# Optimization experiments

Hardware: AMD Instinct MI355X
Metric: run time of the kernel (lower is better)

The kernel has to match this reference:

```python
import jax, jax.numpy as jnp
import numpy as np

N_NODES = 100000


def gcn_conv(x, W, b, src, dst, n):
    """PyG GCNConv: add self-loops, symmetric degree norm, linear, scatter-add."""
    loop = jnp.arange(n, dtype=src.dtype)
    s = jnp.concatenate([src, loop])  # source nodes (message origin)
    d = jnp.concatenate([dst, loop])  # target nodes (aggregation)
    deg = jax.ops.segment_sum(jnp.ones_like(d, dtype=x.dtype), d, num_segments=n)
    dinv = jnp.where(deg > 0, jax.lax.rsqrt(deg), 0.0)
    norm = dinv[s] * dinv[d]  # [E+N]
    h = x @ W  # [N, out]
    msg = h[s] * norm[:, None]  # [E+N, out]
    return jax.ops.segment_sum(msg, d, num_segments=n) + b


def setup_inputs() -> dict:
    key = jax.random.key(0)
    ks = jax.random.split(key, 8)
    n, e, din, dh, dout = N_NODES, 3200000, 128, 64, 6
    x = jax.random.normal(ks[0], (n, din), dtype=jnp.float32)
    edge_index = jax.random.randint(ks[1], (2, e), 0, n, dtype=jnp.int64)
    sc = lambda f: 1.0 / np.sqrt(f)
    W1 = jax.random.normal(ks[2], (din, dh), dtype=jnp.float32) * sc(din)
    b1 = jnp.zeros((dh,), dtype=jnp.float32)
    W2 = jax.random.normal(ks[3], (dh, dh), dtype=jnp.float32) * sc(dh)
    b2 = jnp.zeros((dh,), dtype=jnp.float32)
    W3 = jax.random.normal(ks[4], (dh, dout), dtype=jnp.float32) * sc(dh)
    b3 = jnp.zeros((dout,), dtype=jnp.float32)
    return {"x": x, "edge_index": edge_index, "W1": W1, "b1": b1,
            "W2": W2, "b2": b2, "W3": W3, "b3": b3}


def reference(x, edge_index, W1, b1, W2, b2, W3, b3):
    n = x.shape[0]
    src, dst = edge_index[0], edge_index[1]
    # eval mode: dropout is identity
    h = jax.nn.relu(gcn_conv(x, W1, b1, src, dst, n))
    h = jax.nn.relu(gcn_conv(h, W2, b2, src, dst, n))
    h = gcn_conv(h, W3, b3, src, dst, n)
    return jax.nn.log_softmax(h, axis=1)
```

## Files before the change

### kernel.cpp

```cpp
#include <hip/hip_runtime.h>
#include <hip/hip_fp16.h>
#include <math.h>


#define WS_ALIGN(x) (((x) + 255) & ~(size_t)255)
#define BKN 256
#define CAP 8960
#define EPT 16
#define BIN_THR 512
#define BIN_CHUNK (BIN_THR * EPT)

typedef _Float16 half8 __attribute__((ext_vector_type(8)));
typedef float floatx4 __attribute__((ext_vector_type(4)));

__global__ __launch_bounds__(BIN_THR) void bin_kernel(
    const int* __restrict__ src, const int* __restrict__ dst,
    int* __restrict__ cur, int* __restrict__ slab, int E, int NB) {
    __shared__ int counts[400];
    const int tid = threadIdx.x;
    const int base = blockIdx.x * BIN_CHUNK + tid * EPT;
    for (int i = tid; i < NB; i += BIN_THR) counts[i] = 0;
    __syncthreads();
    int b[EPT], w[EPT], lpos[EPT];
    #pragma unroll
    for (int k = 0; k < EPT; ++k) {
        int e = base + k;
        if (e < E) {
            int s = src[e], d = dst[e];
            b[k] = d >> 8;
            w[k] = (s << 8) | (d & 255);
        } else b[k] = -1;
    }
    #pragma unroll
    for (int k = 0; k < EPT; ++k)
        if (b[k] >= 0) lpos[k] = atomicAdd(&counts[b[k]], 1);
    __syncthreads();
    for (int i = tid; i < NB; i += BIN_THR) {
        int c = counts[i];
        counts[i] = c ? atomicAdd(&cur[i], c) : 0;
    }
    __syncthreads();
    #pragma unroll
    for (int k = 0; k < EPT; ++k) {
        if (b[k] >= 0) {
            int pos = counts[b[k]] + lpos[k];
            if (pos < CAP) slab[(size_t)b[k] * CAP + pos] = w[k];
        }
    }
}

__global__ __launch_bounds__(512) void bucket_sort_kernel(
    const int* __restrict__ slab, const int* __restrict__ cur,
    int* __restrict__ srcS, int* __restrict__ rowbeg, int* __restrict__ rowend,
    float* __restrict__ dinv, int n) {
    __shared__ int cnt[BKN], s[BKN], cursor[BKN];
    const int b = blockIdx.x, tid = threadIdx.x;
    const int m = min(cur[b], CAP);
    const int* sp = slab + (size_t)b * CAP;
    if (tid < BKN) cnt[tid] = 0;
    __syncthreads();
    for (int j = tid; j < m; j += 512) atomicAdd(&cnt[sp[j] & 255], 1);
    __syncthreads();
    if (tid < BKN) s[tid] = cnt[tid];
    __syncthreads();
    for (int off = 1; off < BKN; off <<= 1) {
        int v = 0;
        if (tid < BKN && tid >= off) v = s[tid - off];
        __syncthreads();
        if (tid < BKN) s[tid] += v;
        __syncthreads();
    }
    if (tid < BKN) {
        int ofs = s[tid] - cnt[tid];
        cursor[tid] = ofs;
        int node = b * BKN + tid;
        if (node < n) {
            rowbeg[node] = b * CAP + ofs;
            rowend[node] = b * CAP + ofs + cnt[tid];
            dinv[node] = rsqrtf((float)(cnt[tid] + 1));
        }
    }
    __syncthreads();
    for (int j = tid; j < m; j += 512) {
        int w = sp[j];
        int p = atomicAdd(&cursor[w & 255], 1);
        srcS[(size_t)b * CAP + p] = w >> 8;
    }
}

template <int K>
__global__ __launch_bounds__(256) void linear_mfma_f32_kernel(
    const float* __restrict__ Xf, const float* __restrict__ W,
    const float* __restrict__ dinv, _Float16* __restrict__ Y, int n) {
    constexpr int KC = K / 32;
    __shared__ _Float16 Bf[KC * 4 * 64 * 8];
    const int tid = threadIdx.x;
    for (int i = tid; i < KC * 4 * 64 * 8; i += 256) {
        int j = i & 7, lane = (i >> 3) & 63, tile = (i >> 9) & 3, kc = i >> 11;
        int k = kc * 32 + ((lane >> 4) << 3) + j;
        int col = tile * 16 + (lane & 15);
        Bf[i] = (_Float16)W[k * 64 + col];
    }
    __syncthreads();
    const int lane = tid & 63, wid = tid >> 6;
    const int base = blockIdx.x * 64 + wid * 16;
    if (base >= n) return;
    const int mrow = lane & 15, quad = lane >> 4;
    const int anode = min(base + mrow, n - 1);
    floatx4 acc[4] = {{0, 0, 0, 0}, {0, 0, 0, 0}, {0, 0, 0, 0}, {0, 0, 0, 0}};
    #pragma unroll
    for (int kc = 0; kc < KC; ++kc) {
        float4 xa = *(const float4*)&Xf[(size_t)anode * K + kc * 32 + quad * 8];
        float4 xb = *(const float4*)&Xf[(size_t)anode * K + kc * 32 + quad * 8 + 4];
        half8 a;
        a[0] = (_Float16)xa.x; a[1] = (_Float16)xa.y; a[2] = (_Float16)xa.z; a[3] = (_Float16)xa.w;
        a[4] = (_Float16)xb.x; a[5] = (_Float16)xb.y; a[6] = (_Float16)xb.z; a[7] = (_Float16)xb.w;
        #pragma unroll
        for (int t = 0; t < 4; ++t) {
            half8 b = *(const half8*)&Bf[((kc * 4 + t) * 64 + lane) * 8];
            acc[t] = __builtin_amdgcn_mfma_f32_16x16x32_f16(a, b, acc[t], 0, 0, 0);
        }
    }
    #pragma unroll
    for (int r = 0; r < 4; ++r) {
        int node = base + quad * 4 + r;
        if (node < n) {
            float di = dinv[node];
            #pragma unroll
            for (int t = 0; t < 4; ++t)
                Y[(size_t)node * 64 + t * 16 + mrow] = (_Float16)(acc[t][r] * di);
        }
    }
}

__global__ __launch_bounds__(256) void linear_mfma_f16_kernel(
    const _Float16* __restrict__ Xh, const float* __restrict__ W,
    const float* __restrict__ dinv, _Float16* __restrict__ Y, int n) {
    constexpr int K = 64, KC = 2;
    __shared__ _Float16 Bf[KC * 4 * 64 * 8];
    const int tid = threadIdx.x;
    for (int i = tid; i < KC * 4 * 64 * 8; i += 256) {
        int j = i & 7, lane = (i >> 3) & 63, tile = (i >> 9) & 3, kc = i >> 11;
        int k = kc * 32 + ((lane >> 4) << 3) + j;
        int col = tile * 16 + (lane & 15);
        Bf[i] = (_Float16)W[k * 64 + col];
    }
    __syncthreads();
    const int lane = tid & 63, wid = tid >> 6;
    const int base = blockIdx.x * 64 + wid * 16;
    if (base >= n) return;
    const int mrow = lane & 15, quad = lane >> 4;
    const int anode = min(base + mrow, n - 1);
    floatx4 acc[4] = {{0, 0, 0, 0}, {0, 0, 0, 0}, {0, 0, 0, 0}, {0, 0, 0, 0}};
    #pragma unroll
    for (int kc = 0; kc < KC; ++kc) {
        half8 a = *(const half8*)&Xh[(size_t)anode * K + kc * 32 + quad * 8];
        #pragma unroll
        for (int t = 0; t < 4; ++t) {
            half8 b = *(const half8*)&Bf[((kc * 4 + t) * 64 + lane) * 8];
            acc[t] = __builtin_amdgcn_mfma_f32_16x16x32_f16(a, b, acc[t], 0, 0, 0);
        }
    }
    #pragma unroll
    for (int r = 0; r < 4; ++r) {
        int node = base + quad * 4 + r;
        if (node < n) {
            float di = dinv[node];
            #pragma unroll
            for (int t = 0; t < 4; ++t)
                Y[(size_t)node * 64 + t * 16 + mrow] = (_Float16)(acc[t][r] * di);
        }
    }
}

__global__ __launch_bounds__(256) void linear3_kernel(const __half* __restrict__ Xh,
                                                      const float* __restrict__ W,
                                                      const float* __restrict__ dinv,
                                                      __half* __restrict__ Y, int n) {
    __shared__ float Wl[64 * 6];
    __shared__ float Xs[32][65];
    const int tid = threadIdx.x;
    for (int i = tid; i < 64 * 6; i += 256) Wl[i] = W[i];
    const int sub = tid >> 3;
    const int feat = tid & 7;
    for (int base = blockIdx.x * 32; base < n; base += gridDim.x * 32) {
        __syncthreads();
        for (int i = tid; i < 32 * 64; i += 256) {
            int r = i >> 6, c = i & 63;
            int node = base + r;
            Xs[r][c] = (node < n) ? __half2float(Xh[(size_t)node * 64 + c]) : 0.f;
        }
        __syncthreads();
        int node = base + sub;
        if (node < n) {
            float r = 0.f;
            if (feat < 6) {
                float acc = 0.f;
                #pragma unroll
                for (int k = 0; k < 64; ++k) acc = fmaf(Xs[sub][k], Wl[k * 6 + feat], acc);
                r = acc * dinv[node];
            }
            Y[(size_t)node * 8 + feat] = __float2half_rn(r);
        }
    }
}

__global__ __launch_bounds__(256) void agg64_kernel(
    const _Float16* __restrict__ Hs, const float* __restrict__ dinv,
    const int* __restrict__ srcS, const int* __restrict__ rowbeg,
    const int* __restrict__ rowend, const float* __restrict__ bias,
    _Float16* __restrict__ Out, int n, int do_relu) {
    const int wave = (blockIdx.x * blockDim.x + threadIdx.x) >> 6;
    const int lane = threadIdx.x & 63;
    if (wave >= n) return;
    const int slot = lane >> 3;
    const int f8 = lane & 7;
    const int beg = rowbeg[wave], end = rowend[wave];
    float acc[8] = {0.f, 0.f, 0.f, 0.f, 0.f, 0.f, 0.f, 0.f};
    int j = beg;
    for (; j + 16 <= end; j += 16) {
        int sA = srcS[j + slot];
        int sB = srcS[j + 8 + slot];
        half8 vA = *(const half8*)&Hs[(size_t)sA * 64 + f8 * 8];
        half8 vB = *(const half8*)&Hs[(size_t)sB * 64 + f8 * 8];
        #pragma unroll
        for (int i = 0; i < 8; ++i) acc[i] += (float)vA[i] + (float)vB[i];
    }
    for (; j < end; j += 8) {
        int jj = j + slot;
        int s = srcS[min(jj, end - 1)];
        half8 v = *(const half8*)&Hs[(size_t)s * 64 + f8 * 8];
        float flag = (jj < end) ? 1.f : 0.f;
        #pragma unroll
        for (int i = 0; i < 8; ++i) acc[i] = fmaf((float)v[i], flag, acc[i]);
    }
    #pragma unroll
    for (int i = 0; i < 8; ++i) {
        acc[i] += __shfl_xor(acc[i], 8);
        acc[i] += __shfl_xor(acc[i], 16);
        acc[i] += __shfl_xor(acc[i], 32);
    }
    half8 self = *(const half8*)&Hs[(size_t)wave * 64 + f8 * 8];
    const float di = dinv[wave];
    float4 b0 = *(const float4*)&bias[f8 * 8];
    float4 b1 = *(const float4*)&bias[f8 * 8 + 4];
    float bb[8] = {b0.x, b0.y, b0.z, b0.w, b1.x, b1.y, b1.z, b1.w};
    half8 o;
    #pragma unroll
    for (int i = 0; i < 8; ++i) {
        float v = (acc[i] + (float)self[i]) * di + bb[i];
        if (do_relu) v = fmaxf(v, 0.f);
        o[i] = (_Float16)v;
    }
    if (slot == 0) *(half8*)&Out[(size_t)wave * 64 + f8 * 8] = o;
}

__global__ __launch_bounds__(256) void agg6_lsm_kernel(
    const __half* __restrict__ Hs6, const float* __restrict__ dinv,
    const int* __restrict__ srcS, const int* __restrict__ rowbeg,
    const int* __restrict__ rowend, const float* __restrict__ bias,
    float* __restrict__ out, int n) {
    const int wave = (blockIdx.x * blockDim.x + threadIdx.x) >> 6;
    const int lane = threadIdx.x & 63;
    if (wave >= n) return;
    const int slot = lane >> 3, f = lane & 7;
    const int beg = rowbeg[wave], end = rowend[wave];
    float part = 0.f;
    for (int j0 = beg; j0 < end; j0 += 8) {
        int j = j0 + slot;
        if (j < end) part += __half2float(Hs6[(size_t)srcS[j] * 8 + f]);
    }
    part += __shfl_xor(part, 8);
    part += __shfl_xor(part, 16);
    part += __shfl_xor(part, 32);
    float bi = (f < 6) ? bias[f] : 0.f;
    float a = (part + __half2float(Hs6[(size_t)wave * 8 + f])) * dinv[wave] + bi;
    float am = (f < 6) ? a : -1e30f;
    float m = am;
    m = fmaxf(m, __shfl_xor(m, 1));
    m = fmaxf(m, __shfl_xor(m, 2));
    m = fmaxf(m, __shfl_xor(m, 4));
    float ex = (f < 6) ? expf(a - m) : 0.f;
    float sum = ex;
    sum += __shfl_xor(sum, 1);
    sum += __shfl_xor(sum, 2);
    sum += __shfl_xor(sum, 4);
    float lse = m + logf(sum);
    if (slot == 0 && f < 6) out[(size_t)wave * 6 + f] = a - lse;
}

extern "C" void kernel_launch(void* const* d_in, const int* in_sizes, int n_in,
                              void* d_out, int out_size, void* d_ws, size_t ws_size,
                              hipStream_t stream) {
    const float* x  = (const float*)d_in[0];
    const int*   ei = (const int*)d_in[1];
    const float* W1 = (const float*)d_in[2];
    const float* b1 = (const float*)d_in[3];
    const float* W2 = (const float*)d_in[4];
    const float* b2 = (const float*)d_in[5];
    const float* W3 = (const float*)d_in[6];
    const float* b3 = (const float*)d_in[7];
    float* out = (float*)d_out;

    const int n = in_sizes[0] / 128;
    const int E = in_sizes[1] / 2;
    const int* src = ei;
    const int* dst = ei + E;
    const int NB = (n + BKN - 1) / BKN;

    char* ws = (char*)d_ws;
    auto carve = [&](size_t bytes) { char* p = ws; ws += WS_ALIGN(bytes); return p; };
    int*      cur    = (int*)     carve((size_t)NB * 4);
    float*    dinv   = (float*)   carve((size_t)n * 4);
    int*      slab   = (int*)     carve((size_t)NB * CAP * 4);
    int*      srcS   = (int*)     carve((size_t)NB * CAP * 4);
    int*      rowbeg = (int*)     carve((size_t)n * 4);
    int*      rowend = (int*)     carve((size_t)n * 4);
    _Float16* hsA    = (_Float16*)carve((size_t)n * 64 * 2 + 4096);
    _Float16* hsB    = (_Float16*)carve((size_t)n * 64 * 2 + 4096);
    __half*   hsC    = (__half*)  carve((size_t)n * 8 * 2);
    (void)ws_size; (void)n_in; (void)out_size;

    hipMemsetAsync(cur, 0, (size_t)NB * 4, stream);
    bin_kernel<<<(E + BIN_CHUNK - 1) / BIN_CHUNK, BIN_THR, 0, stream>>>(src, dst, cur, slab, E, NB);
    bucket_sort_kernel<<<NB, 512, 0, stream>>>(slab, cur, srcS, rowbeg, rowend, dinv, n);

    const int aggGrid = (n + 3) / 4;
    const int linGrid = (n + 63) / 64;

    linear_mfma_f32_kernel<128><<<linGrid, 256, 0, stream>>>(x, W1, dinv, hsA, n);
    agg64_kernel<<<aggGrid, 256, 0, stream>>>(hsA, dinv, srcS, rowbeg, rowend, b1, hsB, n, 1);

    linear_mfma_f16_kernel<<<linGrid, 256, 0, stream>>>(hsB, W2, dinv, hsA, n);
    agg64_kernel<<<aggGrid, 256, 0, stream>>>(hsA, dinv, srcS, rowbeg, rowend, b2, hsB, n, 1);

    linear3_kernel<<<2048, 256, 0, stream>>>((const __half*)hsB, W3, dinv, hsC, n);
    agg6_lsm_kernel<<<aggGrid, 256, 0, stream>>>(hsC, dinv, srcS, rowbeg, rowend, b3, out, n);
}
```

Baseline: 374.3 us.

## Fuse layer-3 linear into second aggregation and accumulate gathers in fp16

Removes the separate linear3 kernel by folding the 64x6 projection into the second agg64 pass, using fp16 dot2 on weights staged in LDS plus a lane shuffle reduction. This drops one full read and write of the 64-wide hidden array. The gather accumulation also switches from fp32 to packed fp16 vector adds and fp16 shuffles, which cuts ALU work but lowers accumulation precision for high-degree nodes. The tail loop now uses a branch instead of the masked FMA.

New measurement: 375.1 us. Within noise of the previous version (+0.2%).

```diff
diff --git a/kernel.cpp b/kernel.cpp
--- a/kernel.cpp
+++ b/kernel.cpp
@@ -11,7 +11,21 @@
 #define BIN_CHUNK (BIN_THR * EPT)
 
 typedef _Float16 half8 __attribute__((ext_vector_type(8)));
+typedef _Float16 half2v __attribute__((ext_vector_type(2)));
 typedef float floatx4 __attribute__((ext_vector_type(4)));
+
+#if defined(__has_builtin)
+#if __has_builtin(__builtin_amdgcn_fdot2)
+#define HAVE_FDOT2 1
+#endif
+#endif
+static __device__ __forceinline__ float fdot2f(half2v a, half2v b, float c) {
+#ifdef HAVE_FDOT2
+    return __builtin_amdgcn_fdot2(a, b, c, false);
+#else
+    return c + (float)a[0] * (float)b[0] + (float)a[1] * (float)b[1];
+#endif
+}
 
 __global__ __launch_bounds__(BIN_THR) void bin_kernel(
     const int* __restrict__ src, const int* __restrict__ dst,
@@ -173,86 +187,107 @@
     }
 }
 
-__global__ __launch_bounds__(256) void linear3_kernel(const __half* __restrict__ Xh,
-                                                      const float* __restrict__ W,
-                                                      const float* __restrict__ dinv,
-                                                      __half* __restrict__ Y, int n) {
-    __shared__ float Wl[64 * 6];
-    __shared__ float Xs[32][65];
-    const int tid = threadIdx.x;
-    for (int i = tid; i < 64 * 6; i += 256) Wl[i] = W[i];
-    const int sub = tid >> 3;
-    const int feat = tid & 7;
-    for (int base = blockIdx.x * 32; base < n; base += gridDim.x * 32) {
-        __syncthreads();
-        for (int i = tid; i < 32 * 64; i += 256) {
-            int r = i >> 6, c = i & 63;
-            int node = base + r;
-            Xs[r][c] = (node < n) ? __half2float(Xh[(size_t)node * 64 + c]) : 0.f;
-        }
-        __syncthreads();
-        int node = base + sub;
-        if (node < n) {
-            float r = 0.f;
-            if (feat < 6) {
-                float acc = 0.f;
-                #pragma unroll
-                for (int k = 0; k < 64; ++k) acc = fmaf(Xs[sub][k], Wl[k * 6 + feat], acc);
-                r = acc * dinv[node];
-            }
-            Y[(size_t)node * 8 + feat] = __float2half_rn(r);
-        }
-    }
-}
-
+template <bool FUSE3>
 __global__ __launch_bounds__(256) void agg64_kernel(
     const _Float16* __restrict__ Hs, const float* __restrict__ dinv,
     const int* __restrict__ srcS, const int* __restrict__ rowbeg,
     const int* __restrict__ rowend, const float* __restrict__ bias,
-    _Float16* __restrict__ Out, int n, int do_relu) {
-    const int wave = (blockIdx.x * blockDim.x + threadIdx.x) >> 6;
-    const int lane = threadIdx.x & 63;
+    _Float16* __restrict__ Out, const float* __restrict__ W3,
+    int n, int do_relu) {
+    __shared__ _Float16 W3s[6 * 64];
+    const int tid = threadIdx.x;
+    if (FUSE3) {
+        for (int i = tid; i < 6 * 64; i += 256) {
+            int f = i >> 6, k = i & 63;
+            W3s[i] = (_Float16)W3[k * 6 + f];
+        }
+        __syncthreads();
+    }
+    const int wave = (blockIdx.x * blockDim.x + tid) >> 6;
+    const int lane = tid & 63;
     if (wave >= n) return;
     const int slot = lane >> 3;
     const int f8 = lane & 7;
     const int beg = rowbeg[wave], end = rowend[wave];
-    float acc[8] = {0.f, 0.f, 0.f, 0.f, 0.f, 0.f, 0.f, 0.f};
+    half8 hA, hB;
+    #pragma unroll
+    for (int i = 0; i < 8; ++i) { hA[i] = (_Float16)0.f; hB[i] = (_Float16)0.f; }
     int j = beg;
     for (; j + 16 <= end; j += 16) {
         int sA = srcS[j + slot];
         int sB = srcS[j + 8 + slot];
         half8 vA = *(const half8*)&Hs[(size_t)sA * 64 + f8 * 8];
         half8 vB = *(const half8*)&Hs[(size_t)sB * 64 + f8 * 8];
-        #pragma unroll
-        for (int i = 0; i < 8; ++i) acc[i] += (float)vA[i] + (float)vB[i];
+        hA += vA;
+        hB += vB;
     }
     for (; j < end; j += 8) {
         int jj = j + slot;
-        int s = srcS[min(jj, end - 1)];
-        half8 v = *(const half8*)&Hs[(size_t)s * 64 + f8 * 8];
-        float flag = (jj < end) ? 1.f : 0.f;
-        #pragma unroll
-        for (int i = 0; i < 8; ++i) acc[i] = fmaf((float)v[i], flag, acc[i]);
-    }
-    #pragma unroll
-    for (int i = 0; i < 8; ++i) {
-        acc[i] += __shfl_xor(acc[i], 8);
-        acc[i] += __shfl_xor(acc[i], 16);
-        acc[i] += __shfl_xor(acc[i], 32);
+        if (jj < end) {
+            half8 v = *(const half8*)&Hs[(size_t)srcS[jj] * 64 + f8 * 8];
+            hA += v;
+        }
+    }
+    half8 ht = hA + hB;
+    #pragma unroll
+    for (int mask = 8; mask <= 32; mask <<= 1) {
+        int4 ci = *(int4*)&ht, oi;
+        oi.x = __shfl_xor(ci.x, mask);
+        oi.y = __shfl_xor(ci.y, mask);
+        oi.z = __shfl_xor(ci.z, mask);
+        oi.w = __shfl_xor(ci.w, mask);
+        ht += *(half8*)&oi;
     }
     half8 self = *(const half8*)&Hs[(size_t)wave * 64 + f8 * 8];
     const float di = dinv[wave];
     float4 b0 = *(const float4*)&bias[f8 * 8];
     float4 b1 = *(const float4*)&bias[f8 * 8 + 4];
     float bb[8] = {b0.x, b0.y, b0.z, b0.w, b1.x, b1.y, b1.z, b1.w};
-    half8 o;
+    float v[8];
     #pragma unroll
     for (int i = 0; i < 8; ++i) {
-        float v = (acc[i] + (float)self[i]) * di + bb[i];
-        if (do_relu) v = fmaxf(v, 0.f);
-        o[i] = (_Float16)v;
-    }
-    if (slot == 0) *(half8*)&Out[(size_t)wave * 64 + f8 * 8] = o;
+        float t = ((float)ht[i] + (float)self[i]) * di + bb[i];
+        if (do_relu) t = fmaxf(t, 0.f);
+        v[i] = t;
+    }
+    if (!FUSE3) {
+        half8 o;
+        #pragma unroll
+        for (int i = 0; i < 8; ++i) o[i] = (_Float16)v[i];
+        if (slot == 0) *(half8*)&Out[(size_t)wave * 64 + f8 * 8] = o;
+    } else {
+        half2v vh[4];
+        #pragma unroll
+        for (int p2 = 0; p2 < 4; ++p2) {
+            vh[p2][0] = (_Float16)v[2 * p2];
+            vh[p2][1] = (_Float16)v[2 * p2 + 1];
+        }
+        float p[6];
+        #pragma unroll
+        for (int f = 0; f < 6; ++f) {
+            half8 wv = *(const half8*)&W3s[f * 64 + f8 * 8];
+            const half2v* wp = (const half2v*)&wv;
+            float a = 0.f;
+            a = fdot2f(vh[0], wp[0], a);
+            a = fdot2f(vh[1], wp[1], a);
+            a = fdot2f(vh[2], wp[2], a);
+            a = fdot2f(vh[3], wp[3], a);
+            p[f] = a;
+        }
+        #pragma unroll
+        for (int f = 0; f < 6; ++f) {
+            p[f] += __shfl_xor(p[f], 1);
+            p[f] += __shfl_xor(p[f], 2);
+            p[f] += __shfl_xor(p[f], 4);
+        }
+        if (lane == 0) {
+            half8 o;
+            #pragma unroll
+            for (int f = 0; f < 6; ++f) o[f] = (_Float16)(p[f] * di);
+            o[6] = (_Float16)0.f; o[7] = (_Float16)0.f;
+            *(half8*)&Out[(size_t)wave * 8] = o;
+        }
+    }
 }
 
 __global__ __launch_bounds__(256) void agg6_lsm_kernel(
@@ -318,7 +353,7 @@
     int*      rowend = (int*)     carve((size_t)n * 4);
     _Float16* hsA    = (_Float16*)carve((size_t)n * 64 * 2 + 4096);
     _Float16* hsB    = (_Float16*)carve((size_t)n * 64 * 2 + 4096);
-    __half*   hsC    = (__half*)  carve((size_t)n * 8 * 2);
+    _Float16* hsC    = (_Float16*)carve((size_t)n * 8 * 2);
     (void)ws_size; (void)n_in; (void)out_size;
 
     hipMemsetAsync(cur, 0, (size_t)NB * 4, stream);
@@ -329,11 +364,10 @@
     const int linGrid = (n + 63) / 64;
 
     linear_mfma_f32_kernel<128><<<linGrid, 256, 0, stream>>>(x, W1, dinv, hsA, n);
-    agg64_kernel<<<aggGrid, 256, 0, stream>>>(hsA, dinv, srcS, rowbeg, rowend, b1, hsB, n, 1);
+    agg64_kernel<false><<<aggGrid, 256, 0, stream>>>(hsA, dinv, srcS, rowbeg, rowend, b1, hsB, nullptr, n, 1);
 
     linear_mfma_f16_kernel<<<linGrid, 256, 0, stream>>>(hsB, W2, dinv, hsA, n);
-    agg64_kernel<<<aggGrid, 256, 0, stream>>>(hsA, dinv, srcS, rowbeg, rowend, b2, hsB, n, 1);
-
-    linear3_kernel<<<2048, 256, 0, stream>>>((const __half*)hsB, W3, dinv, hsC, n);
-    agg6_lsm_kernel<<<aggGrid, 256, 0, stream>>>(hsC, dinv, srcS, rowbeg, rowend, b3, out, n);
-}
+    agg64_kernel<true><<<aggGrid, 256, 0, stream>>>(hsA, dinv, srcS, rowbeg, rowend, b2, hsC, W3, n, 1);
+
+    agg6_lsm_kernel<<<aggGrid, 256, 0, stream>>>((const __half*)hsC, dinv, srcS, rowbeg, rowend, b3, out, n);
+}
```
